# Performance work log

Hardware: AMD Instinct MI355X
Metric: run time of the kernel (lower is better)

The kernel has to match this reference:

```python
import jax, jax.numpy as jnp
import numpy as np

NUM_KERNELS = 8
KERNEL_SIZES = [2 ** i for i in range(1, NUM_KERNELS + 1)]


def setup_inputs() -> dict:
    key = jax.random.key(0)
    x = jax.random.uniform(key, (32, 1, 1024, 1024), dtype=jnp.float32)
    return {"x": x}


def _plogp(p):
    # p * log2(p), safely 0 at p == 0 (log2(1) == 0)
    ps = jnp.where(p > 0, p, 1.0)
    return ps * jnp.log2(ps)


def reference(x):
    # Slice_windows(num_kernels=8, mode='entropy', to_binary=False)
    B, C, H, W = x.shape
    cols = []
    for k in KERNEL_SIZES:
        if k > H or k > W:
            cols.append(jnp.zeros((B,), dtype=x.dtype))
            continue
        Hk, Wk = H // k, W // k
        n = k * k * C
        # non-overlapping window sums == sum-pooling with stride k
        xs = x[:, :, : Hk * k, : Wk * k].reshape(B, C, Hk, k, Wk, k)
        s = xs.sum(axis=(1, 3, 5))            # (B, Hk, Wk)
        p1 = s / n
        p0 = 1.0 - p1
        entropy = -_plogp(p0) - _plogp(p1)    # Shannon entropy per window
        cols.append(entropy.mean(axis=(1, 2)))  # average over all windows
    return jnp.stack(cols, axis=1)  # (B, num_kernels)
```

## Files before the change

kernel.cpp:

```cpp
#include <hip/hip_runtime.h>

#define IMG 1024

__device__ __forceinline__ float ent(float s, float inv_n) {
    float p1 = s * inv_n;
    float p0 = 1.0f - p1;
    float l1 = (p1 > 0.0f) ? __log2f(p1) : 0.0f;
    float l0 = (p0 > 0.0f) ? __log2f(p0) : 0.0f;
    return -(p0 * l0 + p1 * l1);
}

__device__ __forceinline__ float bfly_sum(float v) {
#pragma unroll
    for (int m = 32; m >= 1; m >>= 1) v += __shfl_xor(v, m);
    return v;
}

__global__ __launch_bounds__(256, 8) void slice_k1(const float* __restrict__ x,
                                                   float* __restrict__ ws) {
    const int b    = blockIdx.x >> 7;
    const int tile = blockIdx.x & 127;
    const int R = tile >> 2, C = tile & 3;
    const int t = threadIdx.x;
    const int w = t >> 6, l = t & 63;

    const float* p = x + (size_t)b * (IMG * IMG)
                       + (size_t)(R * 32 + w * 8) * IMG + (C * 256 + l * 4);
    float4 v[8];
#pragma unroll
    for (int i = 0; i < 8; ++i)
        v[i] = *(const float4*)(p + (size_t)i * IMG);

    float e2 = 0.f, e4 = 0.f;
    float s4h[4];
#pragma unroll
    for (int i = 0; i < 4; ++i) {
        float4 a = v[2 * i], c = v[2 * i + 1];
        float s2a = a.x + a.y + c.x + c.y;
        float s2b = a.z + a.w + c.z + c.w;
        e2 += ent(s2a, 0.25f) + ent(s2b, 0.25f);
        s4h[i] = s2a + s2b;
    }
    float s4a = s4h[0] + s4h[1], s4b = s4h[2] + s4h[3];
    e4 = ent(s4a, 1.f / 16.f) + ent(s4b, 1.f / 16.f);
    float t8 = s4a + s4b;
    float s8 = t8 + __shfl_xor(t8, 1);
    float e8 = ent(s8, 1.f / 64.f);

    float E2 = bfly_sum(e2), E4 = bfly_sum(e4), E8 = bfly_sum(e8);

    __shared__ float s8l[4][32];
    __shared__ float wle[4][3];
    if ((l & 1) == 0) s8l[w][l >> 1] = s8;
    if (l == 0) { wle[w][0] = E2; wle[w][1] = E4; wle[w][2] = E8 * 0.5f; }
    __syncthreads();

    if (w == 0) {
        int r = (l >> 4) & 1, c = l & 15;
        float s16 = s8l[2 * r][2 * c]     + s8l[2 * r][2 * c + 1]
                  + s8l[2 * r + 1][2 * c] + s8l[2 * r + 1][2 * c + 1];
        float e16 = ent(s16, 1.f / 256.f);
        float u = s16 + __shfl_xor(s16, 1);
        float s32 = u + __shfl_xor(u, 16);
        float e32 = ent(s32, 1.f / 1024.f);
        float E16 = bfly_sum(e16) * 0.5f;
        float E32 = bfly_sum(e32) * 0.125f;
        if (l < 16 && (l & 1) == 0)
            ws[(size_t)b * 1024 + R * 32 + C * 8 + (l >> 1)] = s32;
        if (l == 0) {
            float* rec = ws + 32768 + (size_t)blockIdx.x * 8;
            rec[0] = wle[0][0] + wle[1][0] + wle[2][0] + wle[3][0];
            rec[1] = wle[0][1] + wle[1][1] + wle[2][1] + wle[3][1];
            rec[2] = wle[0][2] + wle[1][2] + wle[2][2] + wle[3][2];
            rec[3] = E16;
            rec[4] = E32;
        }
    }
}

__global__ __launch_bounds__(256) void slice_k2(const float* __restrict__ ws,
                                                float* __restrict__ out) {
    const int b = blockIdx.x, t = threadIdx.x;
    const int w = t >> 6, l = t & 63;

    __shared__ float g[1024];
    ((float4*)g)[t] = ((const float4*)(ws + (size_t)b * 1024))[t];

    float r0 = 0.f, r1 = 0.f, r2 = 0.f, r3 = 0.f, r4 = 0.f;
    if (t < 128) {
        const float* rec = ws + 32768 + ((size_t)(b * 128 + t)) * 8;
        float4 a = *(const float4*)rec;
        r0 = a.x; r1 = a.y; r2 = a.z; r3 = a.w; r4 = rec[4];
    }
    r0 = bfly_sum(r0); r1 = bfly_sum(r1); r2 = bfly_sum(r2);
    r3 = bfly_sum(r3); r4 = bfly_sum(r4);
    __shared__ float wr[4][5];
    __shared__ float w64s[4];
    __shared__ float l64[256];
    if (l == 0) { wr[w][0] = r0; wr[w][1] = r1; wr[w][2] = r2; wr[w][3] = r3; wr[w][4] = r4; }
    __syncthreads();

    int i = t >> 4, j = t & 15;
    float s64 = g[(2 * i) * 32 + 2 * j]     + g[(2 * i) * 32 + 2 * j + 1]
              + g[(2 * i + 1) * 32 + 2 * j] + g[(2 * i + 1) * 32 + 2 * j + 1];
    float e64 = ent(s64, 1.f / 4096.f);
    l64[t] = s64;
    float E64w = bfly_sum(e64);
    if (l == 0) w64s[w] = E64w;
    __syncthreads();

    if (w == 0) {
        int i2 = l >> 3, j2 = l & 7;
        float s128 = l64[(2 * i2) * 16 + 2 * j2]     + l64[(2 * i2) * 16 + 2 * j2 + 1]
                   + l64[(2 * i2 + 1) * 16 + 2 * j2] + l64[(2 * i2 + 1) * 16 + 2 * j2 + 1];
        float e128 = ent(s128, 1.f / 16384.f);
        float E128 = bfly_sum(e128);
        float u = s128 + __shfl_xor(s128, 1);
        float s256 = u + __shfl_xor(u, 8);
        float e256 = ent(s256, 1.f / 65536.f);
        float E256 = bfly_sum(e256) * 0.25f;
        if (l == 0) {
            float E2 = wr[0][0] + wr[1][0] + wr[2][0] + wr[3][0];
            float E4 = wr[0][1] + wr[1][1] + wr[2][1] + wr[3][1];
            float E8 = wr[0][2] + wr[1][2] + wr[2][2] + wr[3][2];
            float E16 = wr[0][3] + wr[1][3] + wr[2][3] + wr[3][3];
            float E32 = wr[0][4] + wr[1][4] + wr[2][4] + wr[3][4];
            float E64 = w64s[0] + w64s[1] + w64s[2] + w64s[3];
            float* o = out + b * 8;
            o[0] = E2  * (1.f / 262144.f);
            o[1] = E4  * (1.f / 65536.f);
            o[2] = E8  * (1.f / 16384.f);
            o[3] = E16 * (1.f / 4096.f);
            o[4] = E32 * (1.f / 1024.f);
            o[5] = E64 * (1.f / 256.f);
            o[6] = E128 * (1.f / 64.f);
            o[7] = E256 * (1.f / 16.f);
        }
    }
}

extern "C" void kernel_launch(void* const* d_in, const int* in_sizes, int n_in,
                              void* d_out, int out_size, void* d_ws, size_t ws_size,
                              hipStream_t stream) {
    const float* x = (const float*)d_in[0];
    float* out = (float*)d_out;
    float* ws  = (float*)d_ws;

    slice_k1<<<32 * 128, 256, 0, stream>>>(x, ws);
    slice_k2<<<32, 256, 0, stream>>>(ws, out);
}
```

Baseline: 185.6 us.

## Process four row strips per block with double-buffered loads in slice_k1

Each block of slice_k1 now covers a 128x256 tile instead of 32x256, so the grid shrinks from 4096 to 1024 blocks. Each warp walks four 8-row strips and prefetches the next strip into a second register buffer while it reduces the current one. The 16- and 32-window sums are now built in registers with shuffles, which removes the shared-memory exchange and the single-warp tail stage, and slice_k2 reads fewer partial records. The cost is more registers per thread (occupancy hint lowered to 4) and fewer blocks in flight to hide memory latency on a bandwidth-bound read of 128 MB.

```diff
diff --git a/kernel.cpp b/kernel.cpp
--- a/kernel.cpp
+++ b/kernel.cpp
@@ -16,65 +16,71 @@
     return v;
 }
 
-__global__ __launch_bounds__(256, 8) void slice_k1(const float* __restrict__ x,
+__global__ __launch_bounds__(256, 4) void slice_k1(const float* __restrict__ x,
                                                    float* __restrict__ ws) {
-    const int b    = blockIdx.x >> 7;
-    const int tile = blockIdx.x & 127;
+    const int b    = blockIdx.x >> 5;
+    const int tile = blockIdx.x & 31;
     const int R = tile >> 2, C = tile & 3;
-    const int t = threadIdx.x;
-    const int w = t >> 6, l = t & 63;
+    const int t = threadIdx.x, w = t >> 6, l = t & 63;
 
     const float* p = x + (size_t)b * (IMG * IMG)
-                       + (size_t)(R * 32 + w * 8) * IMG + (C * 256 + l * 4);
-    float4 v[8];
+                       + (size_t)(R * 128 + w * 32) * IMG + (C * 256 + l * 4);
+
+    float4 buf[2][8];
 #pragma unroll
     for (int i = 0; i < 8; ++i)
-        v[i] = *(const float4*)(p + (size_t)i * IMG);
+        buf[0][i] = *(const float4*)(p + (size_t)i * IMG);
 
-    float e2 = 0.f, e4 = 0.f;
-    float s4h[4];
+    float e2 = 0.f, e4 = 0.f, e8 = 0.f;
+    float s8str[4];
 #pragma unroll
-    for (int i = 0; i < 4; ++i) {
-        float4 a = v[2 * i], c = v[2 * i + 1];
-        float s2a = a.x + a.y + c.x + c.y;
-        float s2b = a.z + a.w + c.z + c.w;
-        e2 += ent(s2a, 0.25f) + ent(s2b, 0.25f);
-        s4h[i] = s2a + s2b;
+    for (int s = 0; s < 4; ++s) {
+        if (s < 3) {
+            const float* q = p + (size_t)(8 * (s + 1)) * IMG;
+#pragma unroll
+            for (int i = 0; i < 8; ++i)
+                buf[(s + 1) & 1][i] = *(const float4*)(q + (size_t)i * IMG);
+        }
+        float4* v = buf[s & 1];
+        float s4h[4];
+#pragma unroll
+        for (int i = 0; i < 4; ++i) {
+            float4 a = v[2 * i], c = v[2 * i + 1];
+            float s2a = a.x + a.y + c.x + c.y;
+            float s2b = a.z + a.w + c.z + c.w;
+            e2 += ent(s2a, 0.25f) + ent(s2b, 0.25f);
+            s4h[i] = s2a + s2b;
+        }
+        float s4a = s4h[0] + s4h[1], s4b = s4h[2] + s4h[3];
+        e4 += ent(s4a, 1.f / 16.f) + ent(s4b, 1.f / 16.f);
+        float t8 = s4a + s4b;
+        float s8 = t8 + __shfl_xor(t8, 1);
+        e8 += ent(s8, 1.f / 64.f);
+        s8str[s] = s8;
     }
-    float s4a = s4h[0] + s4h[1], s4b = s4h[2] + s4h[3];
-    e4 = ent(s4a, 1.f / 16.f) + ent(s4b, 1.f / 16.f);
-    float t8 = s4a + s4b;
-    float s8 = t8 + __shfl_xor(t8, 1);
-    float e8 = ent(s8, 1.f / 64.f);
+    float s16a = s8str[0] + s8str[1]; s16a += __shfl_xor(s16a, 2);
+    float s16b = s8str[2] + s8str[3]; s16b += __shfl_xor(s16b, 2);
+    float e16 = ent(s16a, 1.f / 256.f) + ent(s16b, 1.f / 256.f);
+    float s32 = s16a + s16b; s32 += __shfl_xor(s32, 4);
+    float e32 = ent(s32, 1.f / 1024.f);
+
+    if ((l & 7) == 0)
+        ws[(size_t)b * 1024 + (R * 4 + w) * 32 + C * 8 + (l >> 3)] = s32;
 
     float E2 = bfly_sum(e2), E4 = bfly_sum(e4), E8 = bfly_sum(e8);
+    float E16 = bfly_sum(e16), E32 = bfly_sum(e32);
 
-    __shared__ float s8l[4][32];
-    __shared__ float wle[4][3];
-    if ((l & 1) == 0) s8l[w][l >> 1] = s8;
-    if (l == 0) { wle[w][0] = E2; wle[w][1] = E4; wle[w][2] = E8 * 0.5f; }
+    __shared__ float wle[4][5];
+    if (l == 0) {
+        wle[w][0] = E2; wle[w][1] = E4; wle[w][2] = E8 * 0.5f;
+        wle[w][3] = E16 * 0.25f; wle[w][4] = E32 * 0.125f;
+    }
     __syncthreads();
-
-    if (w == 0) {
-        int r = (l >> 4) & 1, c = l & 15;
-        float s16 = s8l[2 * r][2 * c]     + s8l[2 * r][2 * c + 1]
-                  + s8l[2 * r + 1][2 * c] + s8l[2 * r + 1][2 * c + 1];
-        float e16 = ent(s16, 1.f / 256.f);
-        float u = s16 + __shfl_xor(s16, 1);
-        float s32 = u + __shfl_xor(u, 16);
-        float e32 = ent(s32, 1.f / 1024.f);
-        float E16 = bfly_sum(e16) * 0.5f;
-        float E32 = bfly_sum(e32) * 0.125f;
-        if (l < 16 && (l & 1) == 0)
-            ws[(size_t)b * 1024 + R * 32 + C * 8 + (l >> 1)] = s32;
-        if (l == 0) {
-            float* rec = ws + 32768 + (size_t)blockIdx.x * 8;
-            rec[0] = wle[0][0] + wle[1][0] + wle[2][0] + wle[3][0];
-            rec[1] = wle[0][1] + wle[1][1] + wle[2][1] + wle[3][1];
-            rec[2] = wle[0][2] + wle[1][2] + wle[2][2] + wle[3][2];
-            rec[3] = E16;
-            rec[4] = E32;
-        }
+    if (t == 0) {
+        float* rec = ws + 32768 + (size_t)blockIdx.x * 8;
+#pragma unroll
+        for (int j = 0; j < 5; ++j)
+            rec[j] = wle[0][j] + wle[1][j] + wle[2][j] + wle[3][j];
     }
 }
 
@@ -87,17 +93,17 @@
     ((float4*)g)[t] = ((const float4*)(ws + (size_t)b * 1024))[t];
 
     float r0 = 0.f, r1 = 0.f, r2 = 0.f, r3 = 0.f, r4 = 0.f;
-    if (t < 128) {
-        const float* rec = ws + 32768 + ((size_t)(b * 128 + t)) * 8;
+    if (t < 32) {
+        const float* rec = ws + 32768 + ((size_t)(b * 32 + t)) * 8;
         float4 a = *(const float4*)rec;
         r0 = a.x; r1 = a.y; r2 = a.z; r3 = a.w; r4 = rec[4];
     }
     r0 = bfly_sum(r0); r1 = bfly_sum(r1); r2 = bfly_sum(r2);
     r3 = bfly_sum(r3); r4 = bfly_sum(r4);
-    __shared__ float wr[4][5];
+    __shared__ float wr[5];
     __shared__ float w64s[4];
     __shared__ float l64[256];
-    if (l == 0) { wr[w][0] = r0; wr[w][1] = r1; wr[w][2] = r2; wr[w][3] = r3; wr[w][4] = r4; }
+    if (t == 0) { wr[0] = r0; wr[1] = r1; wr[2] = r2; wr[3] = r3; wr[4] = r4; }
     __syncthreads();
 
     int i = t >> 4, j = t & 15;
@@ -120,19 +126,14 @@
         float e256 = ent(s256, 1.f / 65536.f);
         float E256 = bfly_sum(e256) * 0.25f;
         if (l == 0) {
-            float E2 = wr[0][0] + wr[1][0] + wr[2][0] + wr[3][0];
-            float E4 = wr[0][1] + wr[1][1] + wr[2][1] + wr[3][1];
-            float E8 = wr[0][2] + wr[1][2] + wr[2][2] + wr[3][2];
-            float E16 = wr[0][3] + wr[1][3] + wr[2][3] + wr[3][3];
-            float E32 = wr[0][4] + wr[1][4] + wr[2][4] + wr[3][4];
             float E64 = w64s[0] + w64s[1] + w64s[2] + w64s[3];
             float* o = out + b * 8;
-            o[0] = E2  * (1.f / 262144.f);
-            o[1] = E4  * (1.f / 65536.f);
-            o[2] = E8  * (1.f / 16384.f);
-            o[3] = E16 * (1.f / 4096.f);
-            o[4] = E32 * (1.f / 1024.f);
-            o[5] = E64 * (1.f / 256.f);
+            o[0] = wr[0] * (1.f / 262144.f);
+            o[1] = wr[1] * (1.f / 65536.f);
+            o[2] = wr[2] * (1.f / 16384.f);
+            o[3] = wr[3] * (1.f / 4096.f);
+            o[4] = wr[4] * (1.f / 1024.f);
+            o[5] = E64  * (1.f / 256.f);
             o[6] = E128 * (1.f / 64.f);
             o[7] = E256 * (1.f / 16.f);
         }
@@ -146,6 +147,6 @@
     float* out = (float*)d_out;
     float* ws  = (float*)d_ws;
 
-    slice_k1<<<32 * 128, 256, 0, stream>>>(x, ws);
+    slice_k1<<<32 * 32, 256, 0, stream>>>(x, ws);
     slice_k2<<<32, 256, 0, stream>>>(ws, out);
 }
```

Measured after the change: 192.1 us. +3.5%, slower.
